# Performance work log

Measured on AMD Instinct MI355X. Metric: run time of the kernel, lower is better.

## Reference

```python
import jax, jax.numpy as jnp
import numpy as np
from math import sqrt

EPS = 1e-5
N_BISECT = 30

def _entmax15_impl(x):
    # alpha=1.5 entmax along last axis via bisection (entmax_bisect, alpha=1.5)
    xs = x * 0.5  # (alpha-1) * x
    mx = jnp.max(xs, axis=-1, keepdims=True)
    d = xs.shape[-1]
    lo = mx - 1.0
    hi = mx - d ** -0.5  # d^{-(alpha-1)}
    def body(i, carry):
        lo, hi = carry
        mid = 0.5 * (lo + hi)
        f = jnp.sum(jnp.square(jnp.maximum(xs - mid, 0.0)), -1, keepdims=True) - 1.0
        lo = jnp.where(f > 0, mid, lo)
        hi = jnp.where(f > 0, hi, mid)
        return lo, hi
    lo, hi = jax.lax.fori_loop(0, N_BISECT, body, (lo, hi))
    tau = 0.5 * (lo + hi)
    p = jnp.square(jnp.maximum(xs - tau, 0.0))
    return p / jnp.sum(p, -1, keepdims=True)

@jax.custom_vjp
def entmax15(x):
    return _entmax15_impl(x)

def _entmax15_fwd(x):
    p = _entmax15_impl(x)
    return p, p

def _entmax15_bwd(p, g):
    # exact entmax-1.5 backward (entmax repo): gppr = sqrt(p) on support
    s = jnp.sqrt(p)
    dx = g * s
    q = jnp.sum(dx, -1, keepdims=True) / jnp.sum(s, -1, keepdims=True)
    return (dx - q * s,)

entmax15.defvjp(_entmax15_fwd, _entmax15_bwd)

def layer_norm(x, g, b):
    m = jnp.mean(x, -1, keepdims=True)
    v = jnp.var(x, -1, keepdims=True)
    return (x - m) / jnp.sqrt(v + EPS) * g + b

def mlp(x, w1, b1, w2, b2):
    return jax.nn.gelu(x @ w1 + b1, approximate=False) @ w2 + b2

def hopfield_core(q_in, k_in, H, wq, bq, wk, bk, wv, bv, wo, bo):
    # Faithful to Hopfield.forward with mix=True; `values` arg of the torch
    # module is ignored (it recomputes value_projection(key_projection(keys))).
    B, L, _ = q_in.shape
    S = k_in.shape[1]
    q = (q_in @ wq + bq).reshape(B, L, H, -1)
    k = k_in @ wk + bk
    v = (k @ wv + bv).reshape(B, S, H, -1)
    kh = k.reshape(B, S, H, -1)
    E = q.shape[-1]
    scores = jnp.einsum('blhe,bshe->bhls', q, kh) * (1.0 / sqrt(E))
    A = entmax15(scores)
    out = jnp.einsum('bhls,bshd->blhd', A, v)
    # mix=True: transpose(2,1) then view(B, L, -1) on contiguous (B,H,L,D)
    out = jnp.transpose(out, (0, 2, 1, 3)).reshape(B, L, -1)
    return out @ wo + bo

def _forward(n_heads, x, ct_wq, ct_bq, ct_wk, ct_bk, ct_wv, ct_bv, ct_wo, ct_bo,
             cs_wq, cs_bq, cs_wk, cs_bk, cs_wv, cs_bv, cs_wo, cs_bo, cs_key,
             hp_wq, hp_bq, hp_wk, hp_bk, hp_wv, hp_bv, hp_wo, hp_bo,
             n1_g, n1_b, n2_g, n2_b, n3_g, n3_b, n4_g, n4_b,
             m1_w1, m1_b1, m1_w2, m1_b2, m2_w1, m2_b1, m2_w2, m2_b2):
    b, ts_d, seg, d = x.shape
    time_in = x.reshape(b * ts_d, seg, d)
    time_enc = hopfield_core(time_in, time_in, n_heads,
                             ct_wq, ct_bq, ct_wk, ct_bk, ct_wv, ct_bv, ct_wo, ct_bo)
    dim_in = layer_norm(time_in + time_enc, n1_g, n1_b)
    dim_in = layer_norm(dim_in + mlp(dim_in, m1_w1, m1_b1, m1_w2, m1_b2), n2_g, n2_b)
    # '(b ts_d) seg d -> (b seg) ts_d d'
    series_in = dim_in.reshape(b, ts_d, seg, d).transpose(0, 2, 1, 3).reshape(b * seg, ts_d, d)
    # HopfieldPooling: learned stored patterns as keys
    pooled_keys = jnp.broadcast_to(cs_key, (b * seg,) + cs_key.shape[1:])
    series_h = hopfield_core(series_in, pooled_keys, n_heads,
                             cs_wq, cs_bq, cs_wk, cs_bk, cs_wv, cs_bv, cs_wo, cs_bo)
    pooled_h = hopfield_core(series_in, series_in, n_heads,
                             hp_wq, hp_bq, hp_wk, hp_bk, hp_wv, hp_bv, hp_wo, hp_bo)
    dim_enc = layer_norm(series_h + pooled_h, n3_g, n3_b)
    dim_enc = layer_norm(dim_enc + mlp(dim_enc, m2_w1, m2_b1, m2_w2, m2_b2), n4_g, n4_b)
    # '(b seg) ts_d d -> b ts_d seg d'
    return dim_enc.reshape(b, seg, ts_d, d).transpose(0, 2, 1, 3)

def setup_inputs() -> dict:
    b, ts_d, seg, d, h, dff, factor = 8, 32, 64, 1024, 16, 4096, 10
    keys = iter(jax.random.split(jax.random.key(0), 64))
    def rn(shape, s=0.02):
        return jax.random.normal(next(keys), shape, jnp.float32) * s
    inp = {"x": jax.random.normal(next(keys), (b, ts_d, seg, d), jnp.float32)}
    for p in ("ct", "cs", "hp"):
        inp[p + "_wq"] = rn((d, d)); inp[p + "_bq"] = rn((d,))
        inp[p + "_wk"] = rn((d, d)); inp[p + "_bk"] = rn((d,))
        inp[p + "_wv"] = rn((d, d)); inp[p + "_bv"] = rn((d,))
        inp[p + "_wo"] = rn((d, d)); inp[p + "_bo"] = rn((d,))
    inp["cs_key"] = rn((1, factor, d), 0.1)
    for i in ("1", "2", "3", "4"):
        inp["n" + i + "_g"] = jnp.ones((d,), jnp.float32)
        inp["n" + i + "_b"] = jnp.zeros((d,), jnp.float32)
    for m in ("m1", "m2"):
        inp[m + "_w1"] = rn((d, dff)); inp[m + "_b1"] = rn((dff,))
        inp[m + "_w2"] = rn((dff, d)); inp[m + "_b2"] = rn((d,))
    inp["n_heads"] = h
    return inp

def reference(x, ct_wq, ct_bq, ct_wk, ct_bk, ct_wv, ct_bv, ct_wo, ct_bo,
              cs_wq, cs_bq, cs_wk, cs_bk, cs_wv, cs_bv, cs_wo, cs_bo, cs_key,
              hp_wq, hp_bq, hp_wk, hp_bk, hp_wv, hp_bv, hp_wo, hp_bo,
              n1_g, n1_b, n2_g, n2_b, n3_g, n3_b, n4_g, n4_b,
              m1_w1, m1_b1, m1_w2, m1_b2, m2_w1, m2_b1, m2_w2, m2_b2, n_heads):
    return _forward(n_heads, x, ct_wq, ct_bq, ct_wk, ct_bk, ct_wv, ct_bv, ct_wo, ct_bo,
                    cs_wq, cs_bq, cs_wk, cs_bk, cs_wv, cs_bv, cs_wo, cs_bo, cs_key,
                    hp_wq, hp_bq, hp_wk, hp_bk, hp_wv, hp_bv, hp_wo, hp_bo,
                    n1_g, n1_b, n2_g, n2_b, n3_g, n3_b, n4_g, n4_b,
                    m1_w1, m1_b1, m1_w2, m1_b2, m2_w1, m2_b1, m2_w2, m2_b2)
```

## Files before the change

### kernel.cpp

```cpp
#include <hip/hip_runtime.h>
#include <cstdio>

typedef __bf16 bf16x8 __attribute__((ext_vector_type(8)));
typedef float f32x4 __attribute__((ext_vector_type(4)));
typedef int i32x4 __attribute__((ext_vector_type(4)));
typedef unsigned short u16x4 __attribute__((ext_vector_type(4)));

__device__ __forceinline__ float bf2f(unsigned short u) {
  union { unsigned int i; float f; } x; x.i = ((unsigned int)u) << 16; return x.f;
}
__device__ __forceinline__ unsigned short f2bf(float f) {
  union { float f; unsigned int i; } x; x.f = f;
  unsigned int r = x.i + 0x7fffu + ((x.i >> 16) & 1u);
  return (unsigned short)(r >> 16);
}

__device__ __forceinline__ void gl2lds16(const unsigned short* g, unsigned short* l) {
  __builtin_amdgcn_global_load_lds((const __attribute__((address_space(1))) unsigned int*)g,
                                   (__attribute__((address_space(3))) unsigned int*)l, 16, 0, 0);
}

__global__ __launch_bounds__(256) void k_cast(const float* __restrict__ in,
                                              unsigned short* __restrict__ out, int n4) {
  int i = blockIdx.x * 256 + threadIdx.x;
  if (i >= n4) return;
  f32x4 v = ((const f32x4*)in)[i];
  u16x4 o;
  o[0] = f2bf(v[0]); o[1] = f2bf(v[1]); o[2] = f2bf(v[2]); o[3] = f2bf(v[3]);
  ((u16x4*)out)[i] = o;
}

__global__ __launch_bounds__(256) void k_tcast(const float* __restrict__ src,
                                               unsigned short* __restrict__ dst,
                                               int K, int N) {
  __shared__ float tile[32][33];
  int gx = blockIdx.x * 32;
  int gy = blockIdx.y * 32;
  int t = threadIdx.x;
  int c = t & 31, r0 = t >> 5;
#pragma unroll
  for (int i = 0; i < 4; i++) {
    int r = r0 + i * 8;
    tile[r][c] = src[(size_t)(gy + r) * N + gx + c];
  }
  __syncthreads();
#pragma unroll
  for (int i = 0; i < 4; i++) {
    int r = r0 + i * 8;
    dst[(size_t)(gx + r) * K + gy + c] = f2bf(tile[c][r]);
  }
}

template <bool GELU>
__global__ __launch_bounds__(256) void k_gemm(const unsigned short* __restrict__ A,
                                              const unsigned short* __restrict__ Bt,
                                              const float* __restrict__ bias,
                                              unsigned short* __restrict__ C,
                                              int M, int N, int K) {
  __shared__ unsigned short As[2][128 * 32];
  __shared__ unsigned short Bs[2][128 * 32];
  int nwg = gridDim.x * gridDim.y;
  int lin = blockIdx.y * gridDim.x + blockIdx.x;
  int swz = (nwg & 7) ? lin : ((lin & 7) * (nwg >> 3) + (lin >> 3));
  const int rowA0 = (swz / gridDim.x) * 128, colB0 = (swz % gridDim.x) * 128;
  const int t = threadIdx.x, w = t >> 6, lane = t & 63;
  const int wr = w >> 1, wc = w & 1;
  const int srow = w * 16 + (lane >> 2);
  const int schunk = (lane & 3) ^ ((lane >> 3) & 3);
  const unsigned short* pa = A + (size_t)(rowA0 + srow) * K + schunk * 8;
  const unsigned short* pb = Bt + (size_t)(colB0 + srow) * K + schunk * 8;
  const size_t row64 = (size_t)64 * K;

  f32x4 acc[4][4] = {};
  const int ra = lane & 15;
  const int gp8 = (((lane >> 4) ^ ((ra >> 1) & 3)) * 8);

  auto stage = [&](int buf, int kk) {
    gl2lds16(pa + kk,         &As[buf][w * 512]);
    gl2lds16(pa + row64 + kk, &As[buf][2048 + w * 512]);
    gl2lds16(pb + kk,         &Bs[buf][w * 512]);
    gl2lds16(pb + row64 + kk, &Bs[buf][2048 + w * 512]);
  };
  stage(0, 0);
  int buf = 0;
  for (int kk = 0; kk < K; kk += 32) {
    asm volatile("s_waitcnt vmcnt(0)" ::: "memory");
    __syncthreads();
    if (kk + 32 < K) stage(buf ^ 1, kk + 32);
    bf16x8 af[4], bfr[4];
#pragma unroll
    for (int m = 0; m < 4; m++)
      af[m] = *(const bf16x8*)&As[buf][(wr * 64 + m * 16 + ra) * 32 + gp8];
#pragma unroll
    for (int n = 0; n < 4; n++)
      bfr[n] = *(const bf16x8*)&Bs[buf][(wc * 64 + n * 16 + ra) * 32 + gp8];
#pragma unroll
    for (int m = 0; m < 4; m++)
#pragma unroll
      for (int n = 0; n < 4; n++)
        acc[m][n] = __builtin_amdgcn_mfma_f32_16x16x32_bf16(af[m], bfr[n], acc[m][n], 0, 0, 0);
    buf ^= 1;
  }

  const int cr = (lane >> 4) * 4;
  const int cc = lane & 15;
#pragma unroll
  for (int m = 0; m < 4; m++) {
    int grow = rowA0 + wr * 64 + m * 16 + cr;
#pragma unroll
    for (int n = 0; n < 4; n++) {
      int gcol = colB0 + wc * 64 + n * 16 + cc;
      float bv = bias[gcol];
#pragma unroll
      for (int i = 0; i < 4; i++) {
        float v = acc[m][n][i] + bv;
        if (GELU) v = 0.5f * v * (1.f + erff(v * 0.70710678118654752f));
        C[(size_t)(grow + i) * N + gcol] = f2bf(v);
      }
    }
  }
}

__global__ __launch_bounds__(256) void k_gemm10(const unsigned short* __restrict__ A,
                                                const unsigned short* __restrict__ Bt,
                                                const float* __restrict__ bias,
                                                unsigned short* __restrict__ C) {
  __shared__ float af[1024];
  int m = blockIdx.x, nb = blockIdx.y;
  int t = threadIdx.x;
#pragma unroll
  for (int i = 0; i < 4; i++) af[t * 4 + i] = bf2f(A[(size_t)m * 1024 + t * 4 + i]);
  __syncthreads();
  int w = t >> 6, lane = t & 63;
  for (int n = nb * 64 + w; n < nb * 64 + 64; n += 4) {
    const unsigned short* brow = Bt + (size_t)n * 1024 + lane * 16;
    float acc = 0.f;
#pragma unroll
    for (int j = 0; j < 16; j++) acc += af[lane * 16 + j] * bf2f(brow[j]);
#pragma unroll
    for (int o = 32; o; o >>= 1) acc += __shfl_xor(acc, o);
    if (lane == 0) C[(size_t)m * 1024 + n] = f2bf(acc + bias[n]);
  }
}

template <int L, int S, bool SHARED>
__global__ __launch_bounds__(256) void k_attn(const unsigned short* __restrict__ Q,
                                              const unsigned short* __restrict__ Kb,
                                              const unsigned short* __restrict__ Vb,
                                              unsigned short* __restrict__ Out) {
  constexpr int SP = (S <= 32) ? 32 : 64;
  constexpr int QST = 72;
  constexpr int VST = SP + 8;
  constexpr int CST = SP + 4;
  __shared__ unsigned short Qs[L * QST];
  __shared__ unsigned short Ks[SP * QST];
  __shared__ unsigned short Vt[64 * VST];
  __shared__ float Sc[L * CST];
  __shared__ float Rps[L];
  const int blk = blockIdx.x, batch = blk >> 4, h = blk & 15;
  const int t = threadIdx.x, w = t >> 6, lane = t & 63;

  for (int c = t; c < L * 8; c += 256) {
    int r = c >> 3, ch = (c & 7) * 8;
    *(i32x4*)&Qs[r * QST + ch] =
        *(const i32x4*)&Q[((size_t)(batch * L + r)) * 1024 + h * 64 + ch];
  }
  for (int c = t; c < SP * 8; c += 256) {
    int r = c >> 3, ch = (c & 7) * 8;
    i32x4 v = {0, 0, 0, 0};
    if (r < S) {
      size_t rb = SHARED ? (size_t)r : (size_t)(batch * S + r);
      v = *(const i32x4*)&Kb[rb * 1024 + h * 64 + ch];
    }
    *(i32x4*)&Ks[r * QST + ch] = v;
  }
  for (int c = t; c < SP * 64; c += 256) {
    int s = c >> 6, e = c & 63;
    unsigned short v = 0;
    if (s < S) {
      size_t rb = SHARED ? (size_t)s : (size_t)(batch * S + s);
      v = Vb[rb * 1024 + h * 64 + e];
    }
    Vt[e * VST + s] = v;
  }
  __syncthreads();

  const int ka = (lane >> 4) * 8, ra = lane & 15;
  const int cr = (lane >> 4) * 4, cc = lane & 15;
  constexpr int NT = SP / 16, TT = (L / 16) * NT;
  for (int tt = w; tt < TT; tt += 4) {
    int m = tt / NT, n = tt % NT;
    f32x4 a = {0.f, 0.f, 0.f, 0.f};
#pragma unroll
    for (int ks = 0; ks < 2; ks++) {
      bf16x8 af = *(const bf16x8*)&Qs[(m * 16 + ra) * QST + ks * 32 + ka];
      bf16x8 bf = *(const bf16x8*)&Ks[(n * 16 + ra) * QST + ks * 32 + ka];
      a = __builtin_amdgcn_mfma_f32_16x16x32_bf16(af, bf, a, 0, 0, 0);
    }
#pragma unroll
    for (int i = 0; i < 4; i++)
      Sc[(m * 16 + cr + i) * CST + n * 16 + cc] = a[i] * 0.0625f;
  }
  __syncthreads();

  constexpr int G = 256 / L, RW = 64 / G, SL = SP / G;
  const int row = w * RW + lane / G, sub = lane % G;
  float xs[SL];
#pragma unroll
  for (int j = 0; j < SL; j++) {
    int s = sub * SL + j;
    float v = Sc[row * CST + s];
    if (S < SP && s >= S) v = -1e30f;
    xs[j] = v;
  }
  float mx = xs[0];
#pragma unroll
  for (int j = 1; j < SL; j++) mx = fmaxf(mx, xs[j]);
#pragma unroll
  for (int o = G / 2; o; o >>= 1) mx = fmaxf(mx, __shfl_xor(mx, o));
  const float hoff = (S == 64) ? 0.125f : (S == 32) ? 0.17677669529663687f : 0.31622776601683794f;
  float lo = mx - 1.f, hi = mx - hoff;
#pragma unroll 1
  for (int it = 0; it < 26; it++) {
    float mid = 0.5f * (lo + hi);
    float f = 0.f;
#pragma unroll
    for (int j = 0; j < SL; j++) { float dd = fmaxf(xs[j] - mid, 0.f); f += dd * dd; }
#pragma unroll
    for (int o = G / 2; o; o >>= 1) f += __shfl_xor(f, o);
    bool gt = f > 1.f;
    lo = gt ? mid : lo;
    hi = gt ? hi : mid;
  }
  float tau = 0.5f * (lo + hi);
  float ps = 0.f;
#pragma unroll
  for (int j = 0; j < SL; j++) { float dd = fmaxf(xs[j] - tau, 0.f); xs[j] = dd * dd; ps += xs[j]; }
#pragma unroll
  for (int o = G / 2; o; o >>= 1) ps += __shfl_xor(ps, o);
  if (sub == 0) Rps[row] = 1.f / ps;
  unsigned short* Pb = Qs;
#pragma unroll
  for (int j = 0; j < SL; j += 4) {
    u16x4 pv;
#pragma unroll
    for (int jj = 0; jj < 4; jj++) pv[jj] = f2bf(xs[j + jj]);
    *(u16x4*)&Pb[row * VST + sub * SL + j] = pv;
  }
  __syncthreads();

  constexpr int TT2 = (L / 16) * 4;
  for (int tt = w; tt < TT2; tt += 4) {
    int m = tt >> 2, n = tt & 3;
    f32x4 a = {0.f, 0.f, 0.f, 0.f};
#pragma unroll
    for (int ks = 0; ks < SP / 32; ks++) {
      bf16x8 af = *(const bf16x8*)&Pb[(m * 16 + ra) * VST + ks * 32 + ka];
      bf16x8 bf = *(const bf16x8*)&Vt[(n * 16 + ra) * VST + ks * 32 + ka];
      a = __builtin_amdgcn_mfma_f32_16x16x32_bf16(af, bf, a, 0, 0, 0);
    }
#pragma unroll
    for (int i = 0; i < 4; i++) {
      int l = m * 16 + cr + i, e = n * 16 + cc;
      float val = a[i] * Rps[l];
      int l_new = h * (L / 16) + (l >> 4);
      int cg = (l & 15) * 64 + e;
      Out[((size_t)(batch * L + l_new)) * 1024 + cg] = f2bf(val);
    }
  }
}

template <int MODE, bool F32OUT>
__global__ __launch_bounds__(256) void k_ln(const unsigned short* __restrict__ a,
                                            const unsigned short* __restrict__ b,
                                            const float* __restrict__ g,
                                            const float* __restrict__ be,
                                            void* __restrict__ outp) {
  __shared__ float red[8];
  int r = blockIdx.x, t = threadIdx.x;
  size_t base = (size_t)r * 1024 + t * 4;
  u16x4 av = *(const u16x4*)(a + base);
  u16x4 bv = *(const u16x4*)(b + base);
  float x[4];
  float s = 0.f, ss = 0.f;
#pragma unroll
  for (int i = 0; i < 4; i++) {
    x[i] = bf2f(av[i]) + bf2f(bv[i]);
    s += x[i]; ss += x[i] * x[i];
  }
#pragma unroll
  for (int o = 32; o; o >>= 1) { s += __shfl_xor(s, o); ss += __shfl_xor(ss, o); }
  int w = t >> 6;
  if ((t & 63) == 0) { red[w] = s; red[4 + w] = ss; }
  __syncthreads();
  s = red[0] + red[1] + red[2] + red[3];
  ss = red[4] + red[5] + red[6] + red[7];
  float mean = s * (1.f / 1024.f);
  float var = ss * (1.f / 1024.f) - mean * mean;
  float rstd = rsqrtf(var + 1e-5f);
  int orow;
  if (MODE == 0) orow = r;
  else if (MODE == 1) { int bi = r >> 11, rem = r & 2047; int tt = rem >> 6, sd = rem & 63; orow = (bi << 11) + sd * 32 + tt; }
  else { int bi = r >> 11, rem = r & 2047; int sd = rem >> 5, tt = rem & 31; orow = (bi << 11) + tt * 64 + sd; }
  size_t ob = (size_t)orow * 1024 + t * 4;
  if (F32OUT) {
    f32x4 y;
#pragma unroll
    for (int i = 0; i < 4; i++) y[i] = (x[i] - mean) * rstd * g[t * 4 + i] + be[t * 4 + i];
    *(f32x4*)((float*)outp + ob) = y;
  } else {
    u16x4 y;
#pragma unroll
    for (int i = 0; i < 4; i++) y[i] = f2bf((x[i] - mean) * rstd * g[t * 4 + i] + be[t * 4 + i]);
    *(u16x4*)((unsigned short*)outp + ob) = y;
  }
}


extern "C" void kernel_launch(void* const* d_in, const int* in_sizes, int n_in,
                              void* d_out, int out_size, void* d_ws, size_t ws_size,
                              hipStream_t stream) {
  const int M = 16384;
  if (n_in < 43 || in_sizes[0] != 16777216 || in_sizes[25] != 10240 || in_sizes[34] != 4194304) {
    fprintf(stderr, "kernel_launch: unexpected input layout (n_in=%d s0=%d s25=%d s34=%d)\n",
            n_in, in_sizes[0], n_in > 25 ? in_sizes[25] : -1, n_in > 34 ? in_sizes[34] : -1);
    return;
  }
  const float* x = (const float*)d_in[0];
  const float* w[3][4]; const float* bia[3][4];
  for (int p = 0; p < 3; p++) {
    w[p][0] = (const float*)d_in[1 + 8 * p + 0]; bia[p][0] = (const float*)d_in[1 + 8 * p + 1];
    w[p][1] = (const float*)d_in[1 + 8 * p + 2]; bia[p][1] = (const float*)d_in[1 + 8 * p + 3];
    w[p][2] = (const float*)d_in[1 + 8 * p + 4]; bia[p][2] = (const float*)d_in[1 + 8 * p + 5];
    w[p][3] = (const float*)d_in[1 + 8 * p + 6]; bia[p][3] = (const float*)d_in[1 + 8 * p + 7];
  }
  const float* cs_key = (const float*)d_in[25];
  const float* ng[4]; const float* nb[4];
  for (int i = 0; i < 4; i++) { ng[i] = (const float*)d_in[26 + 2 * i]; nb[i] = (const float*)d_in[27 + 2 * i]; }
  const float* m_w1[2]; const float* m_b1[2]; const float* m_w2[2]; const float* m_b2[2];
  for (int i = 0; i < 2; i++) {
    m_w1[i] = (const float*)d_in[34 + 4 * i]; m_b1[i] = (const float*)d_in[35 + 4 * i];
    m_w2[i] = (const float*)d_in[36 + 4 * i]; m_b2[i] = (const float*)d_in[37 + 4 * i];
  }

  char* base = (char*)d_ws; size_t off = 0;
  auto alloc = [&](size_t bytes) -> void* {
    off = (off + 255) & ~(size_t)255;
    void* p = base + off; off += bytes; return p;
  };
  unsigned short* Wt[3][4];
  for (int p = 0; p < 3; p++)
    for (int j = 0; j < 4; j++) Wt[p][j] = (unsigned short*)alloc((size_t)1024 * 1024 * 2);
  unsigned short* Wm1u = (unsigned short*)alloc((size_t)4096 * 1024 * 2);
  unsigned short* Wm1d = (unsigned short*)alloc((size_t)1024 * 4096 * 2);
  unsigned short* Wm2u = (unsigned short*)alloc((size_t)4096 * 1024 * 2);
  unsigned short* Wm2d = (unsigned short*)alloc((size_t)1024 * 4096 * 2);
  unsigned short* A[5];
  for (int i = 0; i < 5; i++) A[i] = (unsigned short*)alloc((size_t)M * 1024 * 2);
  unsigned short* KeyB = (unsigned short*)alloc((size_t)10 * 1024 * 2);
  unsigned short* Kcs = (unsigned short*)alloc((size_t)10 * 1024 * 2);
  unsigned short* Vcs = (unsigned short*)alloc((size_t)10 * 1024 * 2);
  if (off > ws_size) {
    fprintf(stderr, "kernel_launch: ws too small: need %zu have %zu\n", off, ws_size);
    return;
  }
  const int MC = 8192;
  unsigned short* HbT = A[0];
  unsigned short* HbS = A[1];

  auto gemm = [&](const unsigned short* Ap, const unsigned short* Bt, const float* bi,
                  unsigned short* Cp, int Mm, int Nn, int Kk, bool gelu) {
    dim3 g(Nn / 128, Mm / 128);
    if (gelu) k_gemm<true><<<g, 256, 0, stream>>>(Ap, Bt, bi, Cp, Mm, Nn, Kk);
    else      k_gemm<false><<<g, 256, 0, stream>>>(Ap, Bt, bi, Cp, Mm, Nn, Kk);
  };

  for (int p = 0; p < 3; p++)
    for (int j = 0; j < 4; j++)
      k_tcast<<<dim3(32, 32), 256, 0, stream>>>(w[p][j], Wt[p][j], 1024, 1024);
  k_tcast<<<dim3(128, 32), 256, 0, stream>>>(m_w1[0], Wm1u, 1024, 4096);
  k_tcast<<<dim3(32, 128), 256, 0, stream>>>(m_w2[0], Wm1d, 4096, 1024);
  k_tcast<<<dim3(128, 32), 256, 0, stream>>>(m_w1[1], Wm2u, 1024, 4096);
  k_tcast<<<dim3(32, 128), 256, 0, stream>>>(m_w2[1], Wm2d, 4096, 1024);
  k_cast<<<16384, 256, 0, stream>>>(x, A[0], 16777216 / 4);
  k_cast<<<10, 256, 0, stream>>>(cs_key, KeyB, 10240 / 4);

  gemm(A[0], Wt[0][1], bia[0][1], A[1], M, 1024, 1024, false);
  gemm(A[0], Wt[0][0], bia[0][0], A[2], M, 1024, 1024, false);
  gemm(A[1], Wt[0][2], bia[0][2], A[3], M, 1024, 1024, false);
  k_attn<64, 64, false><<<256 * 16, 256, 0, stream>>>(A[2], A[1], A[3], A[4]);
  gemm(A[4], Wt[0][3], bia[0][3], A[1], M, 1024, 1024, false);
  k_ln<0, false><<<M, 256, 0, stream>>>(A[0], A[1], ng[0], nb[0], A[2]);
  for (int c = 0; c < M; c += MC) {
    gemm(A[2] + (size_t)c * 1024, Wm1u, m_b1[0], HbT, MC, 4096, 1024, true);
    gemm(HbT, Wm1d, m_b2[0], A[4] + (size_t)c * 1024, MC, 1024, 4096, false);
  }
  k_ln<1, false><<<M, 256, 0, stream>>>(A[2], A[4], ng[1], nb[1], A[3]);

  k_gemm10<<<dim3(10, 16), 256, 0, stream>>>(KeyB, Wt[1][1], bia[1][1], Kcs);
  k_gemm10<<<dim3(10, 16), 256, 0, stream>>>(Kcs, Wt[1][2], bia[1][2], Vcs);
  gemm(A[3], Wt[1][0], bia[1][0], A[0], M, 1024, 1024, false);
  k_attn<32, 10, true><<<512 * 16, 256, 0, stream>>>(A[0], Kcs, Vcs, A[1]);
  gemm(A[1], Wt[1][3], bia[1][3], A[2], M, 1024, 1024, false);
  gemm(A[3], Wt[2][1], bia[2][1], A[0], M, 1024, 1024, false);
  gemm(A[3], Wt[2][0], bia[2][0], A[1], M, 1024, 1024, false);
  gemm(A[0], Wt[2][2], bia[2][2], A[4], M, 1024, 1024, false);
  k_attn<32, 32, false><<<512 * 16, 256, 0, stream>>>(A[1], A[0], A[4], A[3]);
  gemm(A[3], Wt[2][3], bia[2][3], A[1], M, 1024, 1024, false);
  k_ln<0, false><<<M, 256, 0, stream>>>(A[2], A[1], ng[2], nb[2], A[0]);
  for (int c = 0; c < M; c += MC) {
    gemm(A[0] + (size_t)c * 1024, Wm2u, m_b1[1], HbS, MC, 4096, 1024, true);
    gemm(HbS, Wm2d, m_b2[1], A[3] + (size_t)c * 1024, MC, 1024, 4096, false);
  }
  k_ln<2, true><<<M, 256, 0, stream>>>(A[0], A[3], ng[3], nb[3], d_out);
}
```

Baseline: 1.654 ms.

## Replace GEMM with 256x256 tiled, 8-wave kernel using interleaved LDS loads and MFMA

Replaces the 128x128, 4-wave, K=32 GEMM with a 512-thread kernel that computes 256x256 tiles (128x256 for the K=4096 down-projections) and uses a K step of 64. The LDS layout uses an XOR swizzle. Fragment loads are split into phases that alternate with MFMA blocks, separated by barriers and s_setprio. The aim is more data reuse per tile and better overlap of LDS reads with matrix math. The costs are more LDS and register pressure, fewer workgroups for the smaller GEMMs, and many extra barriers.

```diff
diff --git a/kernel.cpp b/kernel.cpp
--- a/kernel.cpp
+++ b/kernel.cpp
@@ -51,69 +51,138 @@
   }
 }
 
-template <bool GELU>
-__global__ __launch_bounds__(256) void k_gemm(const unsigned short* __restrict__ A,
-                                              const unsigned short* __restrict__ Bt,
-                                              const float* __restrict__ bias,
-                                              unsigned short* __restrict__ C,
-                                              int M, int N, int K) {
-  __shared__ unsigned short As[2][128 * 32];
-  __shared__ unsigned short Bs[2][128 * 32];
+template <int BM, bool GELU>
+__global__ __launch_bounds__(512, 2) void k_gemm2(const unsigned short* __restrict__ Ag,
+                                                  const unsigned short* __restrict__ Btg,
+                                                  const float* __restrict__ bias,
+                                                  unsigned short* __restrict__ C,
+                                                  int M, int N, int K) {
+  constexpr int RPW = BM / 2;
+  constexpr int RF = RPW / 16;
+  constexpr int RPP = RF / 2;
+  __shared__ unsigned short As[2][BM * 64];
+  __shared__ unsigned short Bs[2][256 * 64];
   int nwg = gridDim.x * gridDim.y;
   int lin = blockIdx.y * gridDim.x + blockIdx.x;
   int swz = (nwg & 7) ? lin : ((lin & 7) * (nwg >> 3) + (lin >> 3));
-  const int rowA0 = (swz / gridDim.x) * 128, colB0 = (swz % gridDim.x) * 128;
+  const int rowA0 = (swz / gridDim.x) * BM, colB0 = (swz % gridDim.x) * 256;
   const int t = threadIdx.x, w = t >> 6, lane = t & 63;
-  const int wr = w >> 1, wc = w & 1;
-  const int srow = w * 16 + (lane >> 2);
-  const int schunk = (lane & 3) ^ ((lane >> 3) & 3);
-  const unsigned short* pa = A + (size_t)(rowA0 + srow) * K + schunk * 8;
-  const unsigned short* pb = Bt + (size_t)(colB0 + srow) * K + schunk * 8;
-  const size_t row64 = (size_t)64 * K;
-
-  f32x4 acc[4][4] = {};
-  const int ra = lane & 15;
-  const int gp8 = (((lane >> 4) ^ ((ra >> 1) & 3)) * 8);
+  const int wm = w >> 2, wn = w & 3;
+  const int g = lane >> 4, ra = lane & 15;
+  const int xorE = (ra & 7) << 3;
+  const int koff0 = (g * 8) ^ xorE;
+  const int koff1 = (32 | (g * 8)) ^ xorE;
+  const int srow8 = lane >> 3;
+  const int scol = ((lane & 7) ^ srow8) * 8;
+
+  f32x4 acc[RF][4] = {};
 
   auto stage = [&](int buf, int kk) {
-    gl2lds16(pa + kk,         &As[buf][w * 512]);
-    gl2lds16(pa + row64 + kk, &As[buf][2048 + w * 512]);
-    gl2lds16(pb + kk,         &Bs[buf][w * 512]);
-    gl2lds16(pb + row64 + kk, &Bs[buf][2048 + w * 512]);
+#pragma unroll
+    for (int i = 0; i < BM / 64; i++) {
+      int rbase = (w + i * 8) * 8;
+      gl2lds16(Ag + (size_t)(rowA0 + rbase + srow8) * K + kk + scol, &As[buf][rbase * 64]);
+    }
+#pragma unroll
+    for (int i = 0; i < 4; i++) {
+      int rbase = (w + i * 8) * 8;
+      gl2lds16(Btg + (size_t)(colB0 + rbase + srow8) * K + kk + scol, &Bs[buf][rbase * 64]);
+    }
   };
+
   stage(0, 0);
+  asm volatile("s_waitcnt vmcnt(0)" ::: "memory");
+  __builtin_amdgcn_s_barrier();
+
+  const int NT = K / 64;
   int buf = 0;
-  for (int kk = 0; kk < K; kk += 32) {
+  bf16x8 afr[RPP][2], bfr[4][2];
+  for (int tt = 0; tt < NT; ++tt) {
+    const unsigned short* Ab = &As[buf][0];
+    const unsigned short* Bb = &Bs[buf][0];
+#pragma unroll
+    for (int r = 0; r < RPP; r++) {
+      int lr = wm * RPW + r * 16 + ra;
+      afr[r][0] = *(const bf16x8*)&Ab[lr * 64 + koff0];
+      afr[r][1] = *(const bf16x8*)&Ab[lr * 64 + koff1];
+    }
+#pragma unroll
+    for (int c = 0; c < 2; c++) {
+      int nr = wn * 64 + c * 16 + ra;
+      bfr[c][0] = *(const bf16x8*)&Bb[nr * 64 + koff0];
+      bfr[c][1] = *(const bf16x8*)&Bb[nr * 64 + koff1];
+    }
+    if (tt + 1 < NT) stage(buf ^ 1, (tt + 1) * 64);
+    __builtin_amdgcn_s_barrier();
+    __builtin_amdgcn_s_setprio(1);
+#pragma unroll
+    for (int r = 0; r < RPP; r++)
+#pragma unroll
+      for (int c = 0; c < 2; c++)
+#pragma unroll
+        for (int ks = 0; ks < 2; ks++)
+          acc[r][c] = __builtin_amdgcn_mfma_f32_16x16x32_bf16(afr[r][ks], bfr[c][ks], acc[r][c], 0, 0, 0);
+    __builtin_amdgcn_s_setprio(0);
+    __builtin_amdgcn_s_barrier();
+#pragma unroll
+    for (int c = 2; c < 4; c++) {
+      int nr = wn * 64 + c * 16 + ra;
+      bfr[c][0] = *(const bf16x8*)&Bb[nr * 64 + koff0];
+      bfr[c][1] = *(const bf16x8*)&Bb[nr * 64 + koff1];
+    }
+    __builtin_amdgcn_s_barrier();
+    __builtin_amdgcn_s_setprio(1);
+#pragma unroll
+    for (int r = 0; r < RPP; r++)
+#pragma unroll
+      for (int c = 2; c < 4; c++)
+#pragma unroll
+        for (int ks = 0; ks < 2; ks++)
+          acc[r][c] = __builtin_amdgcn_mfma_f32_16x16x32_bf16(afr[r][ks], bfr[c][ks], acc[r][c], 0, 0, 0);
+    __builtin_amdgcn_s_setprio(0);
+    __builtin_amdgcn_s_barrier();
+#pragma unroll
+    for (int r = 0; r < RPP; r++) {
+      int lr = wm * RPW + (RPP + r) * 16 + ra;
+      afr[r][0] = *(const bf16x8*)&Ab[lr * 64 + koff0];
+      afr[r][1] = *(const bf16x8*)&Ab[lr * 64 + koff1];
+    }
+    __builtin_amdgcn_s_barrier();
+    __builtin_amdgcn_s_setprio(1);
+#pragma unroll
+    for (int r = 0; r < RPP; r++)
+#pragma unroll
+      for (int c = 0; c < 2; c++)
+#pragma unroll
+        for (int ks = 0; ks < 2; ks++)
+          acc[RPP + r][c] = __builtin_amdgcn_mfma_f32_16x16x32_bf16(afr[r][ks], bfr[c][ks], acc[RPP + r][c], 0, 0, 0);
+    __builtin_amdgcn_s_setprio(0);
+    __builtin_amdgcn_s_barrier();
+    __builtin_amdgcn_s_setprio(1);
+#pragma unroll
+    for (int r = 0; r < RPP; r++)
+#pragma unroll
+      for (int c = 2; c < 4; c++)
+#pragma unroll
+        for (int ks = 0; ks < 2; ks++)
+          acc[RPP + r][c] = __builtin_amdgcn_mfma_f32_16x16x32_bf16(afr[r][ks], bfr[c][ks], acc[RPP + r][c], 0, 0, 0);
+    __builtin_amdgcn_s_setprio(0);
     asm volatile("s_waitcnt vmcnt(0)" ::: "memory");
-    __syncthreads();
-    if (kk + 32 < K) stage(buf ^ 1, kk + 32);
-    bf16x8 af[4], bfr[4];
-#pragma unroll
-    for (int m = 0; m < 4; m++)
-      af[m] = *(const bf16x8*)&As[buf][(wr * 64 + m * 16 + ra) * 32 + gp8];
-#pragma unroll
-    for (int n = 0; n < 4; n++)
-      bfr[n] = *(const bf16x8*)&Bs[buf][(wc * 64 + n * 16 + ra) * 32 + gp8];
-#pragma unroll
-    for (int m = 0; m < 4; m++)
-#pragma unroll
-      for (int n = 0; n < 4; n++)
-        acc[m][n] = __builtin_amdgcn_mfma_f32_16x16x32_bf16(af[m], bfr[n], acc[m][n], 0, 0, 0);
+    __builtin_amdgcn_s_barrier();
     buf ^= 1;
   }
 
-  const int cr = (lane >> 4) * 4;
-  const int cc = lane & 15;
-#pragma unroll
-  for (int m = 0; m < 4; m++) {
-    int grow = rowA0 + wr * 64 + m * 16 + cr;
-#pragma unroll
-    for (int n = 0; n < 4; n++) {
-      int gcol = colB0 + wc * 64 + n * 16 + cc;
+  const int cr = g * 4, cc = ra;
+#pragma unroll
+  for (int r = 0; r < RF; r++) {
+    int grow = rowA0 + wm * RPW + r * 16 + cr;
+#pragma unroll
+    for (int c = 0; c < 4; c++) {
+      int gcol = colB0 + wn * 64 + c * 16 + cc;
       float bv = bias[gcol];
 #pragma unroll
       for (int i = 0; i < 4; i++) {
-        float v = acc[m][n][i] + bv;
+        float v = acc[r][c][i] + bv;
         if (GELU) v = 0.5f * v * (1.f + erff(v * 0.70710678118654752f));
         C[(size_t)(grow + i) * N + gcol] = f2bf(v);
       }
@@ -369,10 +438,16 @@
   unsigned short* HbS = A[1];
 
   auto gemm = [&](const unsigned short* Ap, const unsigned short* Bt, const float* bi,
-                  unsigned short* Cp, int Mm, int Nn, int Kk, bool gelu) {
-    dim3 g(Nn / 128, Mm / 128);
-    if (gelu) k_gemm<true><<<g, 256, 0, stream>>>(Ap, Bt, bi, Cp, Mm, Nn, Kk);
-    else      k_gemm<false><<<g, 256, 0, stream>>>(Ap, Bt, bi, Cp, Mm, Nn, Kk);
+                  unsigned short* Cp, int Mm, int Nn, int Kk, bool gelu, bool bm128) {
+    if (bm128) {
+      dim3 g(Nn / 256, Mm / 128);
+      if (gelu) k_gemm2<128, true><<<g, 512, 0, stream>>>(Ap, Bt, bi, Cp, Mm, Nn, Kk);
+      else      k_gemm2<128, false><<<g, 512, 0, stream>>>(Ap, Bt, bi, Cp, Mm, Nn, Kk);
+    } else {
+      dim3 g(Nn / 256, Mm / 256);
+      if (gelu) k_gemm2<256, true><<<g, 512, 0, stream>>>(Ap, Bt, bi, Cp, Mm, Nn, Kk);
+      else      k_gemm2<256, false><<<g, 512, 0, stream>>>(Ap, Bt, bi, Cp, Mm, Nn, Kk);
+    }
   };
 
   for (int p = 0; p < 3; p++)
@@ -385,32 +460,32 @@
   k_cast<<<16384, 256, 0, stream>>>(x, A[0], 16777216 / 4);
   k_cast<<<10, 256, 0, stream>>>(cs_key, KeyB, 10240 / 4);
 
-  gemm(A[0], Wt[0][1], bia[0][1], A[1], M, 1024, 1024, false);
-  gemm(A[0], Wt[0][0], bia[0][0], A[2], M, 1024, 1024, false);
-  gemm(A[1], Wt[0][2], bia[0][2], A[3], M, 1024, 1024, false);
+  gemm(A[0], Wt[0][1], bia[0][1], A[1], M, 1024, 1024, false, false);
+  gemm(A[0], Wt[0][0], bia[0][0], A[2], M, 1024, 1024, false, false);
+  gemm(A[1], Wt[0][2], bia[0][2], A[3], M, 1024, 1024, false, false);
   k_attn<64, 64, false><<<256 * 16, 256, 0, stream>>>(A[2], A[1], A[3], A[4]);
-  gemm(A[4], Wt[0][3], bia[0][3], A[1], M, 1024, 1024, false);
+  gemm(A[4], Wt[0][3], bia[0][3], A[1], M, 1024, 1024, false, false);
   k_ln<0, false><<<M, 256, 0, stream>>>(A[0], A[1], ng[0], nb[0], A[2]);
   for (int c = 0; c < M; c += MC) {
-    gemm(A[2] + (size_t)c * 1024, Wm1u, m_b1[0], HbT, MC, 4096, 1024, true);
-    gemm(HbT, Wm1d, m_b2[0], A[4] + (size_t)c * 1024, MC, 1024, 4096, false);
+    gemm(A[2] + (size_t)c * 1024, Wm1u, m_b1[0], HbT, MC, 4096, 1024, true, false);
+    gemm(HbT, Wm1d, m_b2[0], A[4] + (size_t)c * 1024, MC, 1024, 4096, false, true);
   }
   k_ln<1, false><<<M, 256, 0, stream>>>(A[2], A[4], ng[1], nb[1], A[3]);
 
   k_gemm10<<<dim3(10, 16), 256, 0, stream>>>(KeyB, Wt[1][1], bia[1][1], Kcs);
   k_gemm10<<<dim3(10, 16), 256, 0, stream>>>(Kcs, Wt[1][2], bia[1][2], Vcs);
-  gemm(A[3], Wt[1][0], bia[1][0], A[0], M, 1024, 1024, false);
+  gemm(A[3], Wt[1][0], bia[1][0], A[0], M, 1024, 1024, false, false);
   k_attn<32, 10, true><<<512 * 16, 256, 0, stream>>>(A[0], Kcs, Vcs, A[1]);
-  gemm(A[1], Wt[1][3], bia[1][3], A[2], M, 1024, 1024, false);
-  gemm(A[3], Wt[2][1], bia[2][1], A[0], M, 1024, 1024, false);
-  gemm(A[3], Wt[2][0], bia[2][0], A[1], M, 1024, 1024, false);
-  gemm(A[0], Wt[2][2], bia[2][2], A[4], M, 1024, 1024, false);
+  gemm(A[1], Wt[1][3], bia[1][3], A[2], M, 1024, 1024, false, false);
+  gemm(A[3], Wt[2][1], bia[2][1], A[0], M, 1024, 1024, false, false);
+  gemm(A[3], Wt[2][0], bia[2][0], A[1], M, 1024, 1024, false, false);
+  gemm(A[0], Wt[2][2], bia[2][2], A[4], M, 1024, 1024, false, false);
   k_attn<32, 32, false><<<512 * 16, 256, 0, stream>>>(A[1], A[0], A[4], A[3]);
-  gemm(A[3], Wt[2][3], bia[2][3], A[1], M, 1024, 1024, false);
+  gemm(A[3], Wt[2][3], bia[2][3], A[1], M, 1024, 1024, false, false);
   k_ln<0, false><<<M, 256, 0, stream>>>(A[2], A[1], ng[2], nb[2], A[0]);
   for (int c = 0; c < M; c += MC) {
-    gemm(A[0] + (size_t)c * 1024, Wm2u, m_b1[1], HbS, MC, 4096, 1024, true);
-    gemm(HbS, Wm2d, m_b2[1], A[3] + (size_t)c * 1024, MC, 1024, 4096, false);
+    gemm(A[0] + (size_t)c * 1024, Wm2u, m_b1[1], HbS, MC, 4096, 1024, true, false);
+    gemm(HbS, Wm2d, m_b2[1], A[3] + (size_t)c * 1024, MC, 1024, 4096, false, true);
   }
   k_ln<2, true><<<M, 256, 0, stream>>>(A[0], A[3], ng[3], nb[3], d_out);
 }
```

New measurement: 1.609 ms. 2.7% less time.
